# Performance work log

Measured on AMD Instinct MI355X. Metric: run time of the kernel, lower is better.

The kernel has to match this reference:

```python
import jax, jax.numpy as jnp
import numpy as np

N = 131072
C = 8
W = 256


def setup_inputs() -> dict:
    key = jax.random.key(0)
    ks = jax.random.split(key, 10)
    s1 = 1.0 / np.sqrt(3.0)
    sw = 1.0 / np.sqrt(W)
    return {
        "positions": jax.random.normal(ks[0], (N, 3), dtype=jnp.float32),
        "times": jax.random.randint(ks[1], (N,), 0, C, dtype=jnp.int64),
        "W1": jax.random.normal(ks[2], (C, 3, W), dtype=jnp.float32) * s1,
        "b1": jnp.zeros((C, W), dtype=jnp.float32),
        "W2": jax.random.normal(ks[3], (C, W, W), dtype=jnp.float32) * sw,
        "b2": jnp.zeros((C, W), dtype=jnp.float32),
        "W3": jax.random.normal(ks[4], (C, W, W), dtype=jnp.float32) * sw,
        "b3": jnp.zeros((C, W), dtype=jnp.float32),
        "W4": jax.random.normal(ks[5], (C, W, 3), dtype=jnp.float32) * sw,
        "b4": jnp.zeros((C, 3), dtype=jnp.float32),
    }


def _mlp(x, w1, c1, w2, c2, w3, c3, w4, c4):
    # 4-layer MLP, Tanh hidden activations and Tanh output activation
    h = jnp.tanh(x @ w1 + c1)
    h = jnp.tanh(h @ w2 + c2)
    h = jnp.tanh(h @ w3 + c3)
    return jnp.tanh(h @ w4 + c4)


def reference(positions, times, W1, b1, W2, b2, W3, b3, W4, b4):
    # offsets = zeros_like(positions); offsets[times==i] = mlp_i(positions[times==i])
    # classes partition the points, so this equals a per-class select-sum.
    offsets = jnp.zeros_like(positions)
    for i in range(C):  # small fixed class count
        out_i = _mlp(positions, W1[i], b1[i], W2[i], b2[i], W3[i], b3[i], W4[i], b4[i])
        mask = (times == i)[:, None]  # [N,1]
        offsets = jnp.where(mask, out_i, offsets)
    return offsets
```

## Files before the change

kernel.cpp:

```cpp
#include <hip/hip_runtime.h>
#include <stdint.h>

#define N_PTS 131072
#define NCLS 8
#define HID 256
#define MT 64
#define CAP 32768

typedef __bf16 bf16x8 __attribute__((ext_vector_type(8)));
typedef float f32x4 __attribute__((ext_vector_type(4)));

__device__ __forceinline__ float tanh_p2(float a) {
  return fmaf(-2.0f, __builtin_amdgcn_rcpf(__expf(a) + 1.0f), 1.0f);
}

__device__ __forceinline__ unsigned short f2bf_rne(float f) {
  unsigned u = __float_as_uint(f);
  u = u + 0x7fffu + ((u >> 16) & 1u);
  return (unsigned short)(u >> 16);
}

__device__ __forceinline__ unsigned pack_bf16(float a, float b) {
  unsigned ua = __float_as_uint(a) + 0x8000u;
  unsigned ub = __float_as_uint(b) + 0x8000u;
  return __builtin_amdgcn_perm(ub, ua, 0x07060302u);
}

#define PK_TILES 256
#define MISC_BLKS 177
#define MISC_N 45184
#define SCAT_BLKS 512
#define PREP_GRID (PK_TILES + MISC_BLKS + SCAT_BLKS)

__global__ __launch_bounds__(256) void k_prep(
    const int* __restrict__ times,
    const float* __restrict__ W1, const float* __restrict__ b1,
    const float* __restrict__ W2, const float* __restrict__ b2,
    const float* __restrict__ W3, const float* __restrict__ b3,
    const float* __restrict__ W4, const float* __restrict__ b4,
    int* __restrict__ hdr, int* __restrict__ sortedIdx,
    unsigned short* __restrict__ packed23,
    float* __restrict__ w1p, float* __restrict__ b2p,
    float* __restrict__ b3p, float* __restrict__ b4p,
    unsigned short* __restrict__ W4p) {
  __shared__ unsigned short T[64][64];
  __shared__ int lh[NCLS], lbase[NCLS];

  int b = blockIdx.x;
  int tid = threadIdx.x;

  if (b < PK_TILES) {
    int cl = b >> 4;
    int l = cl >> 3, c = cl & 7;
    int tile = b & 15;
    int k0 = (tile >> 2) * 64, j0 = (tile & 3) * 64;
    const float* W = (l ? W3 : W2) + c * 65536;
#pragma unroll
    for (int it = 0; it < 4; it++) {
      int f = tid + it * 256;
      int row = f >> 4, cg = f & 15;
      float4 v = *(const float4*)&W[(k0 + row) * 256 + j0 + cg * 4];
      T[row][cg * 4 + 0] = f2bf_rne(2.0f * v.x);
      T[row][cg * 4 + 1] = f2bf_rne(2.0f * v.y);
      T[row][cg * 4 + 2] = f2bf_rne(2.0f * v.z);
      T[row][cg * 4 + 3] = f2bf_rne(2.0f * v.w);
    }
    __syncthreads();
#pragma unroll
    for (int it = 0; it < 2; it++) {
      int g = tid + it * 256;
      int kb = g >> 6, j = g & 63;
      unsigned u[8];
#pragma unroll
      for (int uu = 0; uu < 8; uu++) u[uu] = T[kb * 8 + uu][j];
      uint4 pk = make_uint4(u[0] | (u[1] << 16), u[2] | (u[3] << 16),
                            u[4] | (u[5] << 16), u[6] | (u[7] << 16));
      int base = cl * 65536 + (((k0 >> 3) + kb) * 256 + (j0 + j)) * 8;
      *(uint4*)&packed23[base] = pk;
    }
  } else if (b < PK_TILES + MISC_BLKS) {
    int e2 = (b - PK_TILES) * 256 + tid;
    if (e2 < 8192) {
      int c = e2 >> 10, rem = e2 & 1023;
      int j = rem >> 2, t = rem & 3;
      float v = (t < 3) ? W1[c * 768 + t * 256 + j] : b1[c * 256 + j];
      w1p[e2] = 2.0f * v;
    } else if (e2 < 10240) {
      int i = e2 - 8192;
      b2p[i] = 2.0f * b2[i];
    } else if (e2 < 12288) {
      int i = e2 - 10240;
      b3p[i] = 2.0f * b3[i];
    } else if (e2 < 12416) {
      int i = e2 - 12288;
      int c = i >> 4, r = i & 15;
      b4p[i] = (r < 3) ? 2.0f * b4[c * 3 + r] : 0.0f;
    } else if (e2 < MISC_N) {
      int i = e2 - 12416;
      int c = i >> 12, rem = i & 4095;
      int jj = rem & 7, j = (rem >> 3) & 15, k = ((rem >> 7) << 3) + jj;
      float v = (j < 3) ? 2.0f * W4[c * 768 + k * 3 + j] : 0.0f;
      W4p[c * 4096 + rem] = f2bf_rne(v);
    }
  } else {
    int sb = b - (PK_TILES + MISC_BLKS);
    if (tid < NCLS) lh[tid] = 0;
    __syncthreads();
    int i = sb * 256 + tid;
    int t = times[i];
    int r = atomicAdd(&lh[t], 1);
    __syncthreads();
    if (tid < NCLS) lbase[tid] = lh[tid] ? atomicAdd(&hdr[tid], lh[tid]) : 0;
    __syncthreads();
    sortedIdx[t * CAP + lbase[t] + r] = i;
  }
}

__device__ __forceinline__ void mfma_layer_T(
    unsigned short (*__restrict__ Abuf)[MT][8],
    const unsigned short* __restrict__ Apack,
    const float* __restrict__ biasp,
    int tid) {
  int lane = tid & 63, w = tid >> 6;
  int quad = lane >> 4, l16 = lane & 15;
  int jcol = w * 32 + l16;
  const bf16x8* __restrict__ Af = (const bf16x8*)Apack;

  f32x4 acc[2][4];
#pragma unroll
  for (int jf = 0; jf < 2; jf++) {
    f32x4 bv = *(const f32x4*)&biasp[w * 32 + jf * 16 + quad * 4];
#pragma unroll
    for (int mt = 0; mt < 4; mt++) acc[jf][mt] = bv;
  }

#pragma unroll
  for (int kb = 0; kb < 8; kb++) {
    int kq = kb * 4 + quad;
    bf16x8 af[2], bfr[4];
#pragma unroll
    for (int jf = 0; jf < 2; jf++) af[jf] = Af[kq * 256 + jcol + jf * 16];
#pragma unroll
    for (int mt = 0; mt < 4; mt++)
      bfr[mt] = *(const bf16x8*)&Abuf[kq][mt * 16 + l16][0];
#pragma unroll
    for (int jf = 0; jf < 2; jf++)
#pragma unroll
      for (int mt = 0; mt < 4; mt++)
        acc[jf][mt] = __builtin_amdgcn_mfma_f32_16x16x32_bf16(af[jf], bfr[mt], acc[jf][mt], 0, 0, 0);
  }

  __syncthreads();

#pragma unroll
  for (int jf = 0; jf < 2; jf++) {
    int jbase = w * 32 + jf * 16 + quad * 4;
#pragma unroll
    for (int mt = 0; mt < 4; mt++) {
      float t0 = tanh_p2(acc[jf][mt][0]);
      float t1 = tanh_p2(acc[jf][mt][1]);
      float t2 = tanh_p2(acc[jf][mt][2]);
      float t3 = tanh_p2(acc[jf][mt][3]);
      uint2 pk = make_uint2(pack_bf16(t0, t1), pack_bf16(t2, t3));
      *(uint2*)&Abuf[jbase >> 3][mt * 16 + l16][jbase & 7] = pk;
    }
  }
}

__global__ __launch_bounds__(512, 6) void k_mlp(
    const float* __restrict__ pos,
    const int* __restrict__ hdr, const int* __restrict__ sortedIdx,
    const unsigned short* __restrict__ packed23,
    const float* __restrict__ w1p, const float* __restrict__ b2p,
    const float* __restrict__ b3p, const float* __restrict__ b4p,
    const unsigned short* __restrict__ W4p,
    float* __restrict__ out) {

  __shared__ __align__(16) unsigned short Abuf[32][MT][8];
  __shared__ __align__(16) float4 w1i[256];
  __shared__ __align__(16) float4 xpos4[MT];
  __shared__ int sIdx[MT];

  int b = blockIdx.x;
  int tid = threadIdx.x;

  int c = -1, t0 = 0, cnt = 0;
  {
    int ts = 0;
#pragma unroll
    for (int cc = 0; cc < NCLS; cc++) {
      int cc_cnt = hdr[cc];
      int tiles = (cc_cnt + MT - 1) >> 6;
      if (b >= ts && b < ts + tiles) { c = cc; t0 = b - ts; cnt = cc_cnt; }
      ts += tiles;
    }
  }
  if (c < 0) return;
  int base = c * CAP + t0 * MT;
  int mCount = min(MT, cnt - t0 * MT);

  if (tid < MT) sIdx[tid] = sortedIdx[base + min(tid, mCount - 1)];
  if (tid < 256) w1i[tid] = ((const float4*)(w1p + (size_t)c * 1024))[tid];
  __syncthreads();
  if (tid < MT) {
    int idx = sIdx[tid] * 3;
    xpos4[tid] = make_float4(pos[idx], pos[idx + 1], pos[idx + 2], 0.0f);
  }
  __syncthreads();

  {
    int m = tid & 63, q = tid >> 6;
    float4 xp = xpos4[m];
#pragma unroll
    for (int i8 = 0; i8 < 4; i8++) {
      int j8 = q * 4 + i8;
      unsigned pk[4];
#pragma unroll
      for (int jp = 0; jp < 4; jp++) {
        float t[2];
#pragma unroll
        for (int u = 0; u < 2; u++) {
          float4 wv = w1i[j8 * 8 + jp * 2 + u];
          float a = fmaf(xp.x, wv.x, fmaf(xp.y, wv.y, fmaf(xp.z, wv.z, wv.w)));
          t[u] = tanh_p2(a);
        }
        pk[jp] = pack_bf16(t[0], t[1]);
      }
      *(uint4*)&Abuf[j8][m][0] = make_uint4(pk[0], pk[1], pk[2], pk[3]);
    }
  }
  __syncthreads();

  mfma_layer_T(Abuf, packed23 + ((size_t)c << 16), b2p + c * 256, tid);
  __syncthreads();
  mfma_layer_T(Abuf, packed23 + ((size_t)(8 + c) << 16), b3p + c * 256, tid);
  __syncthreads();

  {
    int lane = tid & 63, w = tid >> 6;
    if (w < 4) {
      int quad = lane >> 4, l16 = lane & 15;
      f32x4 acc = *(const f32x4*)&b4p[c * 16 + quad * 4];
#pragma unroll
      for (int kb = 0; kb < 8; kb++) {
        int kq = kb * 4 + quad;
        bf16x8 a4 = *(const bf16x8*)&W4p[((size_t)c * 512 + kq * 16 + l16) * 8];
        bf16x8 b4f = *(const bf16x8*)&Abuf[kq][w * 16 + l16][0];
        acc = __builtin_amdgcn_mfma_f32_16x16x32_bf16(a4, b4f, acc, 0, 0, 0);
      }
      int m = w * 16 + l16;
      if (quad == 0 && m < mCount) {
        int o = sIdx[m] * 3;
        out[o + 0] = tanh_p2(acc[0]);
        out[o + 1] = tanh_p2(acc[1]);
        out[o + 2] = tanh_p2(acc[2]);
      }
    }
  }
}

extern "C" void kernel_launch(void* const* d_in, const int* in_sizes, int n_in,
                              void* d_out, int out_size, void* d_ws, size_t ws_size,
                              hipStream_t stream) {
  const float* pos = (const float*)d_in[0];
  const int* times = (const int*)d_in[1];
  const float* W1 = (const float*)d_in[2];
  const float* b1 = (const float*)d_in[3];
  const float* W2 = (const float*)d_in[4];
  const float* b2 = (const float*)d_in[5];
  const float* W3 = (const float*)d_in[6];
  const float* b3 = (const float*)d_in[7];
  const float* W4 = (const float*)d_in[8];
  const float* b4 = (const float*)d_in[9];

  char* ws = (char*)d_ws;
  int* hdr = (int*)ws;
  int* sortedIdx = (int*)(ws + 4096);
  float* w1p = (float*)(ws + 1052672);
  float* b2p = (float*)(ws + 1085440);
  float* b3p = (float*)(ws + 1093632);
  float* b4p = (float*)(ws + 1101824);
  unsigned short* W4p = (unsigned short*)(ws + 1102336);
  unsigned short* packed23 = (unsigned short*)(ws + (2u << 20));
  float* out = (float*)d_out;

  hipMemsetAsync(d_ws, 0, 64, stream);
  k_prep<<<PREP_GRID, 256, 0, stream>>>(times, W1, b1, W2, b2, W3, b3, W4, b4,
                                        hdr, sortedIdx, packed23,
                                        w1p, b2p, b3p, b4p, W4p);
  k_mlp<<<N_PTS / MT + NCLS, 512, 0, stream>>>(
      pos, hdr, sortedIdx, packed23, w1p, b2p, b3p, b4p, W4p, out);
}
```

Baseline: 131.3 us.

## Use 128-row tiles with 32x32x16 MFMA and fold exp2 scaling into weights

The point tile per block doubles to 128 rows and the hidden layers move from 16x16x32 to 32x32x16 MFMA. Each wave now computes a 64x64 output block, which reuses each weight fragment across more rows and cuts global weight loads per point. Separately, the tanh scale factor becomes 2/ln2 and is folded into all weights and biases, so tanh can use a native exp2 instead of expf. In exchange, register pressure rises (launch bounds drop to 4 blocks per SM), LDS per block doubles, and the last tile of each class wastes more padded rows.

```diff
diff --git a/kernel.cpp b/kernel.cpp
--- a/kernel.cpp
+++ b/kernel.cpp
@@ -3,15 +3,24 @@
 
 #define N_PTS 131072
 #define NCLS 8
-#define HID 256
-#define MT 64
+#define MT 128
 #define CAP 32768
+#define PS 2.8853900817779268f
 
 typedef __bf16 bf16x8 __attribute__((ext_vector_type(8)));
 typedef float f32x4 __attribute__((ext_vector_type(4)));
+typedef float f32x16 __attribute__((ext_vector_type(16)));
+
+__device__ __forceinline__ float exp2_fast(float a) {
+#if __has_builtin(__builtin_amdgcn_exp2f)
+  return __builtin_amdgcn_exp2f(a);
+#else
+  return exp2f(a);
+#endif
+}
 
 __device__ __forceinline__ float tanh_p2(float a) {
-  return fmaf(-2.0f, __builtin_amdgcn_rcpf(__expf(a) + 1.0f), 1.0f);
+  return fmaf(-2.0f, __builtin_amdgcn_rcpf(exp2_fast(a) + 1.0f), 1.0f);
 }
 
 __device__ __forceinline__ unsigned short f2bf_rne(float f) {
@@ -60,10 +69,10 @@
       int f = tid + it * 256;
       int row = f >> 4, cg = f & 15;
       float4 v = *(const float4*)&W[(k0 + row) * 256 + j0 + cg * 4];
-      T[row][cg * 4 + 0] = f2bf_rne(2.0f * v.x);
-      T[row][cg * 4 + 1] = f2bf_rne(2.0f * v.y);
-      T[row][cg * 4 + 2] = f2bf_rne(2.0f * v.z);
-      T[row][cg * 4 + 3] = f2bf_rne(2.0f * v.w);
+      T[row][cg * 4 + 0] = f2bf_rne(PS * v.x);
+      T[row][cg * 4 + 1] = f2bf_rne(PS * v.y);
+      T[row][cg * 4 + 2] = f2bf_rne(PS * v.z);
+      T[row][cg * 4 + 3] = f2bf_rne(PS * v.w);
     }
     __syncthreads();
 #pragma unroll
@@ -84,22 +93,22 @@
       int c = e2 >> 10, rem = e2 & 1023;
       int j = rem >> 2, t = rem & 3;
       float v = (t < 3) ? W1[c * 768 + t * 256 + j] : b1[c * 256 + j];
-      w1p[e2] = 2.0f * v;
+      w1p[e2] = PS * v;
     } else if (e2 < 10240) {
       int i = e2 - 8192;
-      b2p[i] = 2.0f * b2[i];
+      b2p[i] = PS * b2[i];
     } else if (e2 < 12288) {
       int i = e2 - 10240;
-      b3p[i] = 2.0f * b3[i];
+      b3p[i] = PS * b3[i];
     } else if (e2 < 12416) {
       int i = e2 - 12288;
       int c = i >> 4, r = i & 15;
-      b4p[i] = (r < 3) ? 2.0f * b4[c * 3 + r] : 0.0f;
+      b4p[i] = (r < 3) ? PS * b4[c * 3 + r] : 0.0f;
     } else if (e2 < MISC_N) {
       int i = e2 - 12416;
       int c = i >> 12, rem = i & 4095;
       int jj = rem & 7, j = (rem >> 3) & 15, k = ((rem >> 7) << 3) + jj;
-      float v = (j < 3) ? 2.0f * W4[c * 768 + k * 3 + j] : 0.0f;
+      float v = (j < 3) ? PS * W4[c * 768 + k * 3 + j] : 0.0f;
       W4p[c * 4096 + rem] = f2bf_rne(v);
     }
   } else {
@@ -116,58 +125,66 @@
   }
 }
 
-__device__ __forceinline__ void mfma_layer_T(
+__device__ __forceinline__ void mfma_layer32(
     unsigned short (*__restrict__ Abuf)[MT][8],
     const unsigned short* __restrict__ Apack,
     const float* __restrict__ biasp,
     int tid) {
   int lane = tid & 63, w = tid >> 6;
-  int quad = lane >> 4, l16 = lane & 15;
-  int jcol = w * 32 + l16;
+  int lo = lane & 31, hi = lane >> 5;
+  int jbase = (w & 3) * 64;
+  int mbase = (w >> 2) * 64;
+
+  f32x16 acc[2][2];
+#pragma unroll
+  for (int jt = 0; jt < 2; jt++) {
+#pragma unroll
+    for (int g = 0; g < 4; g++) {
+      f32x4 bv = *(const f32x4*)&biasp[jbase + jt * 32 + g * 8 + hi * 4];
+#pragma unroll
+      for (int r = 0; r < 4; r++) acc[jt][0][g * 4 + r] = bv[r];
+    }
+    acc[jt][1] = acc[jt][0];
+  }
+
   const bf16x8* __restrict__ Af = (const bf16x8*)Apack;
-
-  f32x4 acc[2][4];
-#pragma unroll
-  for (int jf = 0; jf < 2; jf++) {
-    f32x4 bv = *(const f32x4*)&biasp[w * 32 + jf * 16 + quad * 4];
-#pragma unroll
-    for (int mt = 0; mt < 4; mt++) acc[jf][mt] = bv;
-  }
-
-#pragma unroll
-  for (int kb = 0; kb < 8; kb++) {
-    int kq = kb * 4 + quad;
-    bf16x8 af[2], bfr[4];
-#pragma unroll
-    for (int jf = 0; jf < 2; jf++) af[jf] = Af[kq * 256 + jcol + jf * 16];
-#pragma unroll
-    for (int mt = 0; mt < 4; mt++)
-      bfr[mt] = *(const bf16x8*)&Abuf[kq][mt * 16 + l16][0];
-#pragma unroll
-    for (int jf = 0; jf < 2; jf++)
-#pragma unroll
-      for (int mt = 0; mt < 4; mt++)
-        acc[jf][mt] = __builtin_amdgcn_mfma_f32_16x16x32_bf16(af[jf], bfr[mt], acc[jf][mt], 0, 0, 0);
-  }
-
-  __syncthreads();
-
-#pragma unroll
-  for (int jf = 0; jf < 2; jf++) {
-    int jbase = w * 32 + jf * 16 + quad * 4;
-#pragma unroll
-    for (int mt = 0; mt < 4; mt++) {
-      float t0 = tanh_p2(acc[jf][mt][0]);
-      float t1 = tanh_p2(acc[jf][mt][1]);
-      float t2 = tanh_p2(acc[jf][mt][2]);
-      float t3 = tanh_p2(acc[jf][mt][3]);
-      uint2 pk = make_uint2(pack_bf16(t0, t1), pack_bf16(t2, t3));
-      *(uint2*)&Abuf[jbase >> 3][mt * 16 + l16][jbase & 7] = pk;
-    }
-  }
-}
-
-__global__ __launch_bounds__(512, 6) void k_mlp(
+#pragma unroll
+  for (int kq = 0; kq < 16; kq++) {
+    int k8 = kq * 2 + hi;
+    bf16x8 af[2], bfr[2];
+#pragma unroll
+    for (int jt = 0; jt < 2; jt++) af[jt] = Af[k8 * 256 + jbase + jt * 32 + lo];
+#pragma unroll
+    for (int mt = 0; mt < 2; mt++)
+      bfr[mt] = *(const bf16x8*)&Abuf[k8][mbase + mt * 32 + lo][0];
+#pragma unroll
+    for (int jt = 0; jt < 2; jt++)
+#pragma unroll
+      for (int mt = 0; mt < 2; mt++)
+        acc[jt][mt] = __builtin_amdgcn_mfma_f32_32x32x16_bf16(af[jt], bfr[mt], acc[jt][mt], 0, 0, 0);
+  }
+
+  __syncthreads();
+
+#pragma unroll
+  for (int jt = 0; jt < 2; jt++)
+#pragma unroll
+    for (int mt = 0; mt < 2; mt++) {
+      int m = mbase + mt * 32 + lo;
+#pragma unroll
+      for (int g = 0; g < 4; g++) {
+        float t0 = tanh_p2(acc[jt][mt][g * 4 + 0]);
+        float t1 = tanh_p2(acc[jt][mt][g * 4 + 1]);
+        float t2 = tanh_p2(acc[jt][mt][g * 4 + 2]);
+        float t3 = tanh_p2(acc[jt][mt][g * 4 + 3]);
+        uint2 pk = make_uint2(pack_bf16(t0, t1), pack_bf16(t2, t3));
+        int jq = jbase + jt * 32 + g * 8 + hi * 4;
+        *(uint2*)&Abuf[jq >> 3][m][jq & 7] = pk;
+      }
+    }
+}
+
+__global__ __launch_bounds__(512, 4) void k_mlp(
     const float* __restrict__ pos,
     const int* __restrict__ hdr, const int* __restrict__ sortedIdx,
     const unsigned short* __restrict__ packed23,
@@ -190,7 +207,7 @@
 #pragma unroll
     for (int cc = 0; cc < NCLS; cc++) {
       int cc_cnt = hdr[cc];
-      int tiles = (cc_cnt + MT - 1) >> 6;
+      int tiles = (cc_cnt + MT - 1) >> 7;
       if (b >= ts && b < ts + tiles) { c = cc; t0 = b - ts; cnt = cc_cnt; }
       ts += tiles;
     }
@@ -209,11 +226,11 @@
   __syncthreads();
 
   {
-    int m = tid & 63, q = tid >> 6;
+    int m = tid & 127, q = tid >> 7;
     float4 xp = xpos4[m];
 #pragma unroll
-    for (int i8 = 0; i8 < 4; i8++) {
-      int j8 = q * 4 + i8;
+    for (int i8 = 0; i8 < 8; i8++) {
+      int j8 = q * 8 + i8;
       unsigned pk[4];
 #pragma unroll
       for (int jp = 0; jp < 4; jp++) {
@@ -231,30 +248,28 @@
   }
   __syncthreads();
 
-  mfma_layer_T(Abuf, packed23 + ((size_t)c << 16), b2p + c * 256, tid);
-  __syncthreads();
-  mfma_layer_T(Abuf, packed23 + ((size_t)(8 + c) << 16), b3p + c * 256, tid);
+  mfma_layer32(Abuf, packed23 + ((size_t)c << 16), b2p + c * 256, tid);
+  __syncthreads();
+  mfma_layer32(Abuf, packed23 + ((size_t)(8 + c) << 16), b3p + c * 256, tid);
   __syncthreads();
 
   {
     int lane = tid & 63, w = tid >> 6;
-    if (w < 4) {
-      int quad = lane >> 4, l16 = lane & 15;
-      f32x4 acc = *(const f32x4*)&b4p[c * 16 + quad * 4];
-#pragma unroll
-      for (int kb = 0; kb < 8; kb++) {
-        int kq = kb * 4 + quad;
-        bf16x8 a4 = *(const bf16x8*)&W4p[((size_t)c * 512 + kq * 16 + l16) * 8];
-        bf16x8 b4f = *(const bf16x8*)&Abuf[kq][w * 16 + l16][0];
-        acc = __builtin_amdgcn_mfma_f32_16x16x32_bf16(a4, b4f, acc, 0, 0, 0);
-      }
-      int m = w * 16 + l16;
-      if (quad == 0 && m < mCount) {
-        int o = sIdx[m] * 3;
-        out[o + 0] = tanh_p2(acc[0]);
-        out[o + 1] = tanh_p2(acc[1]);
-        out[o + 2] = tanh_p2(acc[2]);
-      }
+    int quad = lane >> 4, l16 = lane & 15;
+    f32x4 acc = *(const f32x4*)&b4p[c * 16 + quad * 4];
+#pragma unroll
+    for (int kb = 0; kb < 8; kb++) {
+      int kq = kb * 4 + quad;
+      bf16x8 a4 = *(const bf16x8*)&W4p[((size_t)c * 512 + kq * 16 + l16) * 8];
+      bf16x8 b4f = *(const bf16x8*)&Abuf[kq][w * 16 + l16][0];
+      acc = __builtin_amdgcn_mfma_f32_16x16x32_bf16(a4, b4f, acc, 0, 0, 0);
+    }
+    int m = w * 16 + l16;
+    if (quad == 0 && m < mCount) {
+      int o = sIdx[m] * 3;
+      out[o + 0] = tanh_p2(acc[0]);
+      out[o + 1] = tanh_p2(acc[1]);
+      out[o + 2] = tanh_p2(acc[2]);
     }
   }
 }
```

Result: slower. 140.3 us (+6.9%).

## Preload layer weights into registers and fold tanh scale into exp2

Applied to the files above, without the earlier changes.

The MLP kernel now loads each wave's whole layer-2 weight fragment set into registers before layer-1 compute. It prefetches the layer-3 fragments while layer 2's epilogue runs, so global weight loads are hidden behind other work instead of sitting inside the MFMA loop. Occupancy is lowered from 6 to 4 waves per SIMD to make room for the extra registers. The weight prescale changes from 2 to 2/ln2 so that tanh can use the native exp2 instruction, and the weight packing kernel drops its LDS transpose in favour of direct strided loads.

```diff
diff --git a/kernel.cpp b/kernel.cpp
--- a/kernel.cpp
+++ b/kernel.cpp
@@ -3,15 +3,23 @@
 
 #define N_PTS 131072
 #define NCLS 8
-#define HID 256
 #define MT 64
 #define CAP 32768
+#define PS 2.8853900817779268f
 
 typedef __bf16 bf16x8 __attribute__((ext_vector_type(8)));
 typedef float f32x4 __attribute__((ext_vector_type(4)));
 
+__device__ __forceinline__ float exp2_fast(float a) {
+#if __has_builtin(__builtin_amdgcn_exp2f)
+  return __builtin_amdgcn_exp2f(a);
+#else
+  return exp2f(a);
+#endif
+}
+
 __device__ __forceinline__ float tanh_p2(float a) {
-  return fmaf(-2.0f, __builtin_amdgcn_rcpf(__expf(a) + 1.0f), 1.0f);
+  return fmaf(-2.0f, __builtin_amdgcn_rcpf(exp2_fast(a) + 1.0f), 1.0f);
 }
 
 __device__ __forceinline__ unsigned short f2bf_rne(float f) {
@@ -26,11 +34,11 @@
   return __builtin_amdgcn_perm(ub, ua, 0x07060302u);
 }
 
-#define PK_TILES 256
+#define PK2_BLKS 512
 #define MISC_BLKS 177
 #define MISC_N 45184
 #define SCAT_BLKS 512
-#define PREP_GRID (PK_TILES + MISC_BLKS + SCAT_BLKS)
+#define PREP_GRID (PK2_BLKS + MISC_BLKS + SCAT_BLKS)
 
 __global__ __launch_bounds__(256) void k_prep(
     const int* __restrict__ times,
@@ -43,67 +51,51 @@
     float* __restrict__ w1p, float* __restrict__ b2p,
     float* __restrict__ b3p, float* __restrict__ b4p,
     unsigned short* __restrict__ W4p) {
-  __shared__ unsigned short T[64][64];
   __shared__ int lh[NCLS], lbase[NCLS];
 
   int b = blockIdx.x;
   int tid = threadIdx.x;
 
-  if (b < PK_TILES) {
-    int cl = b >> 4;
+  if (b < PK2_BLKS) {
+    int cl = b >> 5;
+    int k8 = b & 31;
+    int j = tid;
     int l = cl >> 3, c = cl & 7;
-    int tile = b & 15;
-    int k0 = (tile >> 2) * 64, j0 = (tile & 3) * 64;
-    const float* W = (l ? W3 : W2) + c * 65536;
-#pragma unroll
-    for (int it = 0; it < 4; it++) {
-      int f = tid + it * 256;
-      int row = f >> 4, cg = f & 15;
-      float4 v = *(const float4*)&W[(k0 + row) * 256 + j0 + cg * 4];
-      T[row][cg * 4 + 0] = f2bf_rne(2.0f * v.x);
-      T[row][cg * 4 + 1] = f2bf_rne(2.0f * v.y);
-      T[row][cg * 4 + 2] = f2bf_rne(2.0f * v.z);
-      T[row][cg * 4 + 3] = f2bf_rne(2.0f * v.w);
-    }
-    __syncthreads();
-#pragma unroll
-    for (int it = 0; it < 2; it++) {
-      int g = tid + it * 256;
-      int kb = g >> 6, j = g & 63;
-      unsigned u[8];
-#pragma unroll
-      for (int uu = 0; uu < 8; uu++) u[uu] = T[kb * 8 + uu][j];
-      uint4 pk = make_uint4(u[0] | (u[1] << 16), u[2] | (u[3] << 16),
-                            u[4] | (u[5] << 16), u[6] | (u[7] << 16));
-      int base = cl * 65536 + (((k0 >> 3) + kb) * 256 + (j0 + j)) * 8;
-      *(uint4*)&packed23[base] = pk;
-    }
-  } else if (b < PK_TILES + MISC_BLKS) {
-    int e2 = (b - PK_TILES) * 256 + tid;
+    const float* W = (l ? W3 : W2) + c * 65536 + k8 * 8 * 256 + j;
+    float v0 = W[0],        v1 = W[256],     v2 = W[2 * 256], v3 = W[3 * 256];
+    float v4 = W[4 * 256],  v5 = W[5 * 256], v6 = W[6 * 256], v7 = W[7 * 256];
+    uint4 pk;
+    pk.x = (unsigned)f2bf_rne(PS * v0) | ((unsigned)f2bf_rne(PS * v1) << 16);
+    pk.y = (unsigned)f2bf_rne(PS * v2) | ((unsigned)f2bf_rne(PS * v3) << 16);
+    pk.z = (unsigned)f2bf_rne(PS * v4) | ((unsigned)f2bf_rne(PS * v5) << 16);
+    pk.w = (unsigned)f2bf_rne(PS * v6) | ((unsigned)f2bf_rne(PS * v7) << 16);
+    *(uint4*)&packed23[cl * 65536 + (k8 * 256 + j) * 8] = pk;
+  } else if (b < PK2_BLKS + MISC_BLKS) {
+    int e2 = (b - PK2_BLKS) * 256 + tid;
     if (e2 < 8192) {
       int c = e2 >> 10, rem = e2 & 1023;
       int j = rem >> 2, t = rem & 3;
       float v = (t < 3) ? W1[c * 768 + t * 256 + j] : b1[c * 256 + j];
-      w1p[e2] = 2.0f * v;
+      w1p[e2] = PS * v;
     } else if (e2 < 10240) {
       int i = e2 - 8192;
-      b2p[i] = 2.0f * b2[i];
+      b2p[i] = PS * b2[i];
     } else if (e2 < 12288) {
       int i = e2 - 10240;
-      b3p[i] = 2.0f * b3[i];
+      b3p[i] = PS * b3[i];
     } else if (e2 < 12416) {
       int i = e2 - 12288;
       int c = i >> 4, r = i & 15;
-      b4p[i] = (r < 3) ? 2.0f * b4[c * 3 + r] : 0.0f;
+      b4p[i] = (r < 3) ? PS * b4[c * 3 + r] : 0.0f;
     } else if (e2 < MISC_N) {
       int i = e2 - 12416;
       int c = i >> 12, rem = i & 4095;
       int jj = rem & 7, j = (rem >> 3) & 15, k = ((rem >> 7) << 3) + jj;
-      float v = (j < 3) ? 2.0f * W4[c * 768 + k * 3 + j] : 0.0f;
+      float v = (j < 3) ? PS * W4[c * 768 + k * 3 + j] : 0.0f;
       W4p[c * 4096 + rem] = f2bf_rne(v);
     }
   } else {
-    int sb = b - (PK_TILES + MISC_BLKS);
+    int sb = b - (PK2_BLKS + MISC_BLKS);
     if (tid < NCLS) lh[tid] = 0;
     __syncthreads();
     int i = sb * 256 + tid;
@@ -116,15 +108,17 @@
   }
 }
 
-__device__ __forceinline__ void mfma_layer_T(
+template <bool PRELOAD_NEXT>
+__device__ __forceinline__ void mfma_layer16(
     unsigned short (*__restrict__ Abuf)[MT][8],
-    const unsigned short* __restrict__ Apack,
+    bf16x8 (&af)[2][8],
+    bf16x8 (&afn)[2][8],
+    const bf16x8* __restrict__ nextAf,
     const float* __restrict__ biasp,
     int tid) {
   int lane = tid & 63, w = tid >> 6;
   int quad = lane >> 4, l16 = lane & 15;
   int jcol = w * 32 + l16;
-  const bf16x8* __restrict__ Af = (const bf16x8*)Apack;
 
   f32x4 acc[2][4];
 #pragma unroll
@@ -137,9 +131,7 @@
 #pragma unroll
   for (int kb = 0; kb < 8; kb++) {
     int kq = kb * 4 + quad;
-    bf16x8 af[2], bfr[4];
-#pragma unroll
-    for (int jf = 0; jf < 2; jf++) af[jf] = Af[kq * 256 + jcol + jf * 16];
+    bf16x8 bfr[4];
 #pragma unroll
     for (int mt = 0; mt < 4; mt++)
       bfr[mt] = *(const bf16x8*)&Abuf[kq][mt * 16 + l16][0];
@@ -147,10 +139,18 @@
     for (int jf = 0; jf < 2; jf++)
 #pragma unroll
       for (int mt = 0; mt < 4; mt++)
-        acc[jf][mt] = __builtin_amdgcn_mfma_f32_16x16x32_bf16(af[jf], bfr[mt], acc[jf][mt], 0, 0, 0);
-  }
-
-  __syncthreads();
+        acc[jf][mt] = __builtin_amdgcn_mfma_f32_16x16x32_bf16(af[jf][kb], bfr[mt], acc[jf][mt], 0, 0, 0);
+  }
+
+  __syncthreads();
+
+  if (PRELOAD_NEXT) {
+#pragma unroll
+    for (int jf = 0; jf < 2; jf++)
+#pragma unroll
+      for (int kb = 0; kb < 8; kb++)
+        afn[jf][kb] = nextAf[(kb * 4 + quad) * 256 + jcol + jf * 16];
+  }
 
 #pragma unroll
   for (int jf = 0; jf < 2; jf++) {
@@ -167,7 +167,7 @@
   }
 }
 
-__global__ __launch_bounds__(512, 6) void k_mlp(
+__global__ __launch_bounds__(512, 4) void k_mlp(
     const float* __restrict__ pos,
     const int* __restrict__ hdr, const int* __restrict__ sortedIdx,
     const unsigned short* __restrict__ packed23,
@@ -198,6 +198,19 @@
   if (c < 0) return;
   int base = c * CAP + t0 * MT;
   int mCount = min(MT, cnt - t0 * MT);
+
+  int lane = tid & 63, w = tid >> 6;
+  int quad = lane >> 4, l16 = lane & 15;
+  int jcol = w * 32 + l16;
+
+  const bf16x8* Af2 = (const bf16x8*)(packed23 + ((size_t)c << 16));
+  const bf16x8* Af3 = (const bf16x8*)(packed23 + ((size_t)(8 + c) << 16));
+  bf16x8 afA[2][8], afB[2][8];
+#pragma unroll
+  for (int jf = 0; jf < 2; jf++)
+#pragma unroll
+    for (int kb = 0; kb < 8; kb++)
+      afA[jf][kb] = Af2[(kb * 4 + quad) * 256 + jcol + jf * 16];
 
   if (tid < MT) sIdx[tid] = sortedIdx[base + min(tid, mCount - 1)];
   if (tid < 256) w1i[tid] = ((const float4*)(w1p + (size_t)c * 1024))[tid];
@@ -231,30 +244,26 @@
   }
   __syncthreads();
 
-  mfma_layer_T(Abuf, packed23 + ((size_t)c << 16), b2p + c * 256, tid);
-  __syncthreads();
-  mfma_layer_T(Abuf, packed23 + ((size_t)(8 + c) << 16), b3p + c * 256, tid);
-  __syncthreads();
-
-  {
-    int lane = tid & 63, w = tid >> 6;
-    if (w < 4) {
-      int quad = lane >> 4, l16 = lane & 15;
-      f32x4 acc = *(const f32x4*)&b4p[c * 16 + quad * 4];
-#pragma unroll
-      for (int kb = 0; kb < 8; kb++) {
-        int kq = kb * 4 + quad;
-        bf16x8 a4 = *(const bf16x8*)&W4p[((size_t)c * 512 + kq * 16 + l16) * 8];
-        bf16x8 b4f = *(const bf16x8*)&Abuf[kq][w * 16 + l16][0];
-        acc = __builtin_amdgcn_mfma_f32_16x16x32_bf16(a4, b4f, acc, 0, 0, 0);
-      }
-      int m = w * 16 + l16;
-      if (quad == 0 && m < mCount) {
-        int o = sIdx[m] * 3;
-        out[o + 0] = tanh_p2(acc[0]);
-        out[o + 1] = tanh_p2(acc[1]);
-        out[o + 2] = tanh_p2(acc[2]);
-      }
+  mfma_layer16<true>(Abuf, afA, afB, Af3, b2p + c * 256, tid);
+  __syncthreads();
+  mfma_layer16<false>(Abuf, afB, afA, nullptr, b3p + c * 256, tid);
+  __syncthreads();
+
+  if (w < 4) {
+    f32x4 acc = *(const f32x4*)&b4p[c * 16 + quad * 4];
+#pragma unroll
+    for (int kb = 0; kb < 8; kb++) {
+      int kq = kb * 4 + quad;
+      bf16x8 a4 = *(const bf16x8*)&W4p[((size_t)c * 512 + kq * 16 + l16) * 8];
+      bf16x8 b4f = *(const bf16x8*)&Abuf[kq][w * 16 + l16][0];
+      acc = __builtin_amdgcn_mfma_f32_16x16x32_bf16(a4, b4f, acc, 0, 0, 0);
+    }
+    int m = w * 16 + l16;
+    if (quad == 0 && m < mCount) {
+      int o = sIdx[m] * 3;
+      out[o + 0] = tanh_p2(acc[0]);
+      out[o + 1] = tanh_p2(acc[1]);
+      out[o + 2] = tanh_p2(acc[2]);
     }
   }
 }
```

After: 140.3 us. 6.9% more time.
